# Optimization experiments

Hardware: AMD Instinct MI355X
Metric: run time of the kernel (lower is better)

The kernel has to match this reference:

```python
import jax, jax.numpy as jnp
import numpy as np

B, T, D = 4, 2048, 1024
H, Dh = 16, 64
Q_LAT, KV_LAT, O_LAT = 512, 256, 512
ROPE = 32
FFN_RANK, FFN_INTER = 384, 4096
EPS = 1e-6
THETA = 10000.0


def rms_norm(x, w, eps=EPS):
    xf = x.astype(jnp.float32)
    var = jnp.mean(xf * xf, axis=-1, keepdims=True)
    return (w * (xf * jax.lax.rsqrt(var + eps))).astype(x.dtype)


def rotate_half(x):
    x1, x2 = jnp.split(x, 2, axis=-1)
    return jnp.concatenate([-x2, x1], axis=-1)


def setup_inputs() -> dict:
    key = jax.random.key(0)
    ks = jax.random.split(key, 12)
    s = lambda fan_in: 1.0 / np.sqrt(fan_in)
    inp = {
        "hidden_states": jax.random.normal(ks[0], (B, T, D), jnp.float32),
        "ln1_w": jnp.ones((D,), jnp.float32),
        "a_ln_w": jnp.ones((Q_LAT + KV_LAT,), jnp.float32),
        "qkv_a_w": jax.random.normal(ks[1], (D, Q_LAT + KV_LAT), jnp.float32) * s(D),
        "q_b_w": jax.random.normal(ks[2], (Q_LAT, H * Dh), jnp.float32) * s(Q_LAT),
        "kv_b_w": jax.random.normal(ks[3], (KV_LAT, 2 * H * Dh), jnp.float32) * s(KV_LAT),
        "o_a_w": jax.random.normal(ks[4], (H * Dh, O_LAT), jnp.float32) * s(H * Dh),
        "o_b_w": jax.random.normal(ks[5], (O_LAT, D), jnp.float32) * s(O_LAT),
        "ln2_w": jnp.ones((D,), jnp.float32),
        "ffn_in_a": jax.random.normal(ks[6], (D, FFN_RANK), jnp.float32) * s(D),
        "ffn_in_b": jax.random.normal(ks[7], (FFN_RANK, FFN_INTER), jnp.float32) * s(FFN_RANK),
        "ffn_out_a": jax.random.normal(ks[8], (FFN_INTER, FFN_RANK), jnp.float32) * s(FFN_INTER),
        "ffn_out_b": jax.random.normal(ks[9], (FFN_RANK, D), jnp.float32) * s(FFN_RANK),
    }
    # RoPE tables over first ROPE dims of each head
    inv_freq = 1.0 / (THETA ** (np.arange(0, ROPE, 2, dtype=np.float32) / ROPE))
    t = np.arange(T, dtype=np.float32)
    freqs = np.outer(t, inv_freq)                      # [T, ROPE/2]
    emb = np.concatenate([freqs, freqs], axis=-1)      # [T, ROPE]
    inp["cos"] = jnp.asarray(np.cos(emb), jnp.float32)
    inp["sin"] = jnp.asarray(np.sin(emb), jnp.float32)
    return inp


def reference(hidden_states, cos, sin, ln1_w, a_ln_w, qkv_a_w, q_b_w, kv_b_w,
              o_a_w, o_b_w, ln2_w, ffn_in_a, ffn_in_b, ffn_out_a, ffn_out_b):
    x = hidden_states
    # --- MLA attention (pre-norm) ---
    h = rms_norm(x, ln1_w)
    lat = rms_norm(h @ qkv_a_w, a_ln_w)                # [B,T,Q_LAT+KV_LAT]
    q_lat, kv_lat = jnp.split(lat, [Q_LAT], axis=-1)
    q = (q_lat @ q_b_w).reshape(B, T, H, Dh).transpose(0, 2, 1, 3)   # [B,H,T,Dh]
    kv = (kv_lat @ kv_b_w).reshape(B, T, H, 2 * Dh).transpose(0, 2, 1, 3)
    k, v = jnp.split(kv, 2, axis=-1)
    # partial RoPE on first ROPE dims
    c = cos[None, None]; s_ = sin[None, None]          # [1,1,T,ROPE]
    q_r, q_p = q[..., :ROPE], q[..., ROPE:]
    k_r, k_p = k[..., :ROPE], k[..., ROPE:]
    q = jnp.concatenate([q_r * c + rotate_half(q_r) * s_, q_p], axis=-1)
    k = jnp.concatenate([k_r * c + rotate_half(k_r) * s_, k_p], axis=-1)
    scores = jnp.einsum("bhqd,bhkd->bhqk", q, k) * (Dh ** -0.5)
    attn = jax.nn.softmax(scores, axis=-1)
    ctx = jnp.einsum("bhqk,bhkd->bhqd", attn, v)
    ctx = ctx.transpose(0, 2, 1, 3).reshape(B, T, H * Dh)
    attn_out = (ctx @ o_a_w) @ o_b_w                   # output subspace
    x = x + attn_out
    # --- decomposed FFN (pre-norm) ---
    h2 = rms_norm(x, ln2_w)
    ff = jax.nn.gelu((h2 @ ffn_in_a) @ ffn_in_b)
    ff = (ff @ ffn_out_a) @ ffn_out_b
    return x + ff
```

## Files before the change

### kernel.cpp

```cpp
#include <hip/hip_runtime.h>
#include <hip/hip_bf16.h>
#include <stdint.h>

#define NTOK 8192

typedef unsigned short u16;
typedef __attribute__((ext_vector_type(4))) float f32x4;
typedef __attribute__((ext_vector_type(8))) short s16x8;
typedef __attribute__((ext_vector_type(4))) short s16x4;
typedef __attribute__((ext_vector_type(8))) u16   u16x8;
typedef __attribute__((ext_vector_type(4))) u16   u16x4;
typedef __attribute__((ext_vector_type(4))) uint32_t u32x4;

__device__ __forceinline__ float fast_exp2(float x) {
    return __builtin_amdgcn_exp2f(x);
}
__device__ __forceinline__ u16 f2bf(float f) {
    uint32_t u = __float_as_uint(f);
    u = (u + 0x7FFFu + ((u >> 16) & 1u)) >> 16;
    return (u16)u;
}
__device__ __forceinline__ float bf2f(u16 h) {
    return __uint_as_float(((uint32_t)h) << 16);
}
__device__ __forceinline__ void async_cp16(const void* g, void* l) {
    __builtin_amdgcn_global_load_lds(
        (const __attribute__((address_space(1))) void*)g,
        (__attribute__((address_space(3))) void*)l, 16, 0, 0);
}
__device__ __forceinline__ void wait_vm4()   { asm volatile("s_waitcnt vmcnt(4)" ::: "memory"); }
__device__ __forceinline__ void wait_vm0()   { asm volatile("s_waitcnt vmcnt(0)" ::: "memory"); }
__device__ __forceinline__ void wait_lgkm0() { asm volatile("s_waitcnt lgkmcnt(0)" ::: "memory"); }
__device__ __forceinline__ void raw_barrier(){ asm volatile("s_barrier" ::: "memory"); }

struct TDesc { const float* s; u16* d; int K; int N; int tile0; };
struct TPack { TDesc t[8]; };

__global__ __launch_bounds__(256) void k_transpose_all(TPack p)
{
    __shared__ float tile[32][33];
    int bid = blockIdx.x;
    int i = 0;
    #pragma unroll
    for (int j = 1; j < 8; j++) if (bid >= p.t[j].tile0) i = j;
    const float* src = p.t[i].s;
    u16* dst = p.t[i].d;
    int K = p.t[i].K, N = p.t[i].N;
    int local = bid - p.t[i].tile0;
    int nx = N >> 5;
    int n0 = (local % nx) * 32, k0 = (local / nx) * 32;
    int tx = threadIdx.x, ty = threadIdx.y;
    #pragma unroll
    for (int r = 0; r < 32; r += 8)
        tile[ty + r][tx] = src[(size_t)(k0 + ty + r) * N + n0 + tx];
    __syncthreads();
    #pragma unroll
    for (int r = 0; r < 32; r += 8)
        dst[(size_t)(n0 + ty + r) * K + k0 + tx] = f2bf(tile[tx][ty + r]);
}

__global__ __launch_bounds__(256) void k_cvt(
    const float* __restrict__ in, u16* __restrict__ out)
{
    int i = (blockIdx.x * 256 + threadIdx.x) * 4;
    f32x4 v = *(const f32x4*)&in[i];
    u16x4 o;
    #pragma unroll
    for (int j = 0; j < 4; j++) o[j] = f2bf(v[j]);
    *(u16x4*)&out[i] = o;
}

template<int W>
__global__ __launch_bounds__(256) void k_rmsnorm(
    const float* __restrict__ x, const float* __restrict__ w, u16* __restrict__ out)
{
    constexpr int E = W / 256;
    int row = blockIdx.x, tid = threadIdx.x;
    const float* xr = x + (size_t)row * W;
    float v[E]; float ss = 0.f;
    #pragma unroll
    for (int i = 0; i < E; i++) { v[i] = xr[tid + i * 256]; ss += v[i] * v[i]; }
    #pragma unroll
    for (int m = 1; m < 64; m <<= 1) ss += __shfl_xor(ss, m, 64);
    __shared__ float red[4];
    if ((tid & 63) == 0) red[tid >> 6] = ss;
    __syncthreads();
    ss = red[0] + red[1] + red[2] + red[3];
    float scale = rsqrtf(ss / (float)W + 1e-6f);
    u16* orow = out + (size_t)row * W;
    #pragma unroll
    for (int i = 0; i < E; i++)
        orow[tid + i * 256] = f2bf(w[tid + i * 256] * (v[i] * scale));
}

template<int EPI>
__global__ __launch_bounds__(256) void k_gemm(
    const u16* __restrict__ A, int lda,
    const u16* __restrict__ Bt, int ldb,
    int M, int N, int K,
    float* __restrict__ outF, u16* __restrict__ outB,
    const float* __restrict__ resid)
{
    __shared__ __align__(16) u16 As[2][4096];
    __shared__ __align__(16) u16 Bs[2][4096];
    int tid = threadIdx.x;
    int w = tid >> 6, lane = tid & 63;
    int m0 = blockIdx.y * 128, n0 = blockIdx.x * 128;
    int wm = w & 1, wn = w >> 1;
    int lr = lane & 15, lq = lane >> 4;

    f32x4 acc[4][4];
    #pragma unroll
    for (int i = 0; i < 4; i++)
        #pragma unroll
        for (int j = 0; j < 4; j++) acc[i][j] = (f32x4)(0.f);

    int ar = tid >> 2;
    int ac = (tid & 3) * 8;
    const u16* Ag = A  + (size_t)(m0 + ar) * lda + ac;
    const u16* Bg = Bt + (size_t)(n0 + ar) * ldb + ac;
    int lo = w * 512;

    auto stage = [&](int kt, int s) {
        const u16* a  = Ag + kt * 32;
        const u16* bp = Bg + kt * 32;
        async_cp16(a,                     &As[s][lo]);
        async_cp16(a + (size_t)64 * lda,  &As[s][lo + 2048]);
        async_cp16(bp,                    &Bs[s][lo]);
        async_cp16(bp + (size_t)64 * ldb, &Bs[s][lo + 2048]);
    };

    int nk = K >> 5;
    stage(0, 0);
    stage(1, 1);
    for (int k = 0; k < nk; k++) {
        if (k + 1 < nk) wait_vm4(); else wait_vm0();
        raw_barrier();
        int s = k & 1;
        s16x8 af[4], bfr[4];
        #pragma unroll
        for (int ms = 0; ms < 4; ms++)
            af[ms] = *reinterpret_cast<const s16x8*>(&As[s][(wm * 64 + ms * 16 + lr) * 32 + lq * 8]);
        #pragma unroll
        for (int ns = 0; ns < 4; ns++)
            bfr[ns] = *reinterpret_cast<const s16x8*>(&Bs[s][(wn * 64 + ns * 16 + lr) * 32 + lq * 8]);
        #pragma unroll
        for (int ms = 0; ms < 4; ms++)
            #pragma unroll
            for (int ns = 0; ns < 4; ns++)
                acc[ms][ns] = __builtin_amdgcn_mfma_f32_16x16x32_bf16(af[ms], bfr[ns], acc[ms][ns], 0, 0, 0);
        wait_lgkm0();
        raw_barrier();
        if (k + 2 < nk) stage(k + 2, s);
    }

    #pragma unroll
    for (int ms = 0; ms < 4; ms++) {
        #pragma unroll
        for (int ns = 0; ns < 4; ns++) {
            int col = n0 + wn * 64 + ns * 16 + lr;
            #pragma unroll
            for (int r = 0; r < 4; r++) {
                int row = m0 + wm * 64 + ms * 16 + lq * 4 + r;
                float v = acc[ms][ns][r];
                size_t idx = (size_t)row * N + col;
                if (EPI == 0) {
                    outF[idx] = v;
                } else if (EPI == 1) {
                    outB[idx] = f2bf(v);
                } else if (EPI == 2) {
                    float t = 0.7978845608028654f * (v + 0.044715f * v * v * v);
                    outB[idx] = f2bf(0.5f * v * (1.f + tanhf(t)));
                } else {
                    outF[idx] = v + resid[idx];
                }
            }
        }
    }
}

template<int EPI>
__global__ __launch_bounds__(256) void k_gemm64(
    const u16* __restrict__ A, int lda,
    const u16* __restrict__ Bt, int ldb,
    int M, int N, int K,
    float* __restrict__ outF, u16* __restrict__ outB)
{
    __shared__ __align__(16) u16 As[2][4096];
    __shared__ __align__(16) u16 Bs[2][4096];
    int tid = threadIdx.x;
    int w = tid >> 6, lane = tid & 63;
    int m0 = blockIdx.y * 64, n0 = blockIdx.x * 64;
    int wm = w & 1, wn = w >> 1;
    int lr = lane & 15, lq = lane >> 4;

    f32x4 acc[2][2];
    #pragma unroll
    for (int i = 0; i < 2; i++)
        #pragma unroll
        for (int j = 0; j < 2; j++) acc[i][j] = (f32x4)(0.f);

    int srow = tid >> 2;
    int sq   = tid & 3;
    const u16* Ag = A  + (size_t)(m0 + srow) * lda + sq * 8;
    const u16* Bg = Bt + (size_t)(n0 + srow) * ldb + sq * 8;
    int lo = srow * 32 + sq * 8;

    auto stage = [&](int kt, int s) {
        const u16* a  = Ag + kt * 64;
        const u16* bp = Bg + kt * 64;
        async_cp16(a,       &As[s][lo]);
        async_cp16(a + 32,  &As[s][2048 + lo]);
        async_cp16(bp,      &Bs[s][lo]);
        async_cp16(bp + 32, &Bs[s][2048 + lo]);
    };

    int nk = K >> 6;
    stage(0, 0);
    stage(1, 1);
    for (int k = 0; k < nk; k++) {
        if (k + 1 < nk) wait_vm4(); else wait_vm0();
        raw_barrier();
        int s = k & 1;
        s16x8 af[2][2], bfr[2][2];
        #pragma unroll
        for (int kc = 0; kc < 2; kc++) {
            #pragma unroll
            for (int ms = 0; ms < 2; ms++)
                af[ms][kc] = *reinterpret_cast<const s16x8*>(
                    &As[s][kc * 2048 + (wm * 32 + ms * 16 + lr) * 32 + lq * 8]);
            #pragma unroll
            for (int ns = 0; ns < 2; ns++)
                bfr[ns][kc] = *reinterpret_cast<const s16x8*>(
                    &Bs[s][kc * 2048 + (wn * 32 + ns * 16 + lr) * 32 + lq * 8]);
        }
        #pragma unroll
        for (int kc = 0; kc < 2; kc++)
            #pragma unroll
            for (int ms = 0; ms < 2; ms++)
                #pragma unroll
                for (int ns = 0; ns < 2; ns++)
                    acc[ms][ns] = __builtin_amdgcn_mfma_f32_16x16x32_bf16(
                        af[ms][kc], bfr[ns][kc], acc[ms][ns], 0, 0, 0);
        wait_lgkm0();
        raw_barrier();
        if (k + 2 < nk) stage(k + 2, s);
    }

    #pragma unroll
    for (int ms = 0; ms < 2; ms++) {
        #pragma unroll
        for (int ns = 0; ns < 2; ns++) {
            int col = n0 + wn * 32 + ns * 16 + lr;
            #pragma unroll
            for (int r = 0; r < 4; r++) {
                int row = m0 + wm * 32 + ms * 16 + lq * 4 + r;
                float v = acc[ms][ns][r];
                size_t idx = (size_t)row * N + col;
                if (EPI == 0) outF[idx] = v;
                else          outB[idx] = f2bf(v);
            }
        }
    }
}

__global__ __launch_bounds__(256) void k_rope(
    const u16* __restrict__ q, const u16* __restrict__ kv,
    const float* __restrict__ cosb, const float* __restrict__ sinb,
    u16* __restrict__ q_r, u16* __restrict__ k_r)
{
    const float QS = 0.125f * 1.4426950408889634f;
    int idx = blockIdx.x * 256 + threadIdx.x;
    int g = idx & 7;
    int h = (idx >> 3) & 15;
    int t = (idx >> 7) & 2047;
    int b = idx >> 18;
    size_t qsrc = ((size_t)((b * 2048 + t) * 16 + h)) * 64 + g * 8;
    size_t ksrc = ((size_t)((b * 2048 + t) * 16 + h)) * 128 + g * 8;
    u16x8 qa = *(const u16x8*)&q[qsrc];
    u16x8 ka = *(const u16x8*)&kv[ksrc];
    u16x8 qo, ko;
    if (g < 4) {
        int pd = ((g ^ 2) - g) * 8;
        u16x8 qp = *(const u16x8*)&q[qsrc + pd];
        u16x8 kp = *(const u16x8*)&kv[ksrc + pd];
        float sgn = (g < 2) ? -1.f : 1.f;
        const float* cp = &cosb[t * 32 + g * 8];
        const float* sp = &sinb[t * 32 + g * 8];
        #pragma unroll
        for (int j = 0; j < 8; j++) {
            float c = cp[j], s = sp[j];
            qo[j] = f2bf((bf2f(qa[j]) * c + sgn * bf2f(qp[j]) * s) * QS);
            ko[j] = f2bf(bf2f(ka[j]) * c + sgn * bf2f(kp[j]) * s);
        }
    } else {
        #pragma unroll
        for (int j = 0; j < 8; j++) {
            qo[j] = f2bf(bf2f(qa[j]) * QS);
            ko[j] = ka[j];
        }
    }
    size_t dst = ((size_t)(b * 16 + h) * 2048 + t) * 64 + g * 8;
    *(u16x8*)&q_r[dst] = qo;
    *(u16x8*)&k_r[dst] = ko;
}

__global__ __launch_bounds__(256) void k_vtrans(
    const u16* __restrict__ kv, u16* __restrict__ v_t)
{
    __shared__ u16 tile[64][72];
    int bh = blockIdx.y;
    int b = bh >> 4, h = bh & 15;
    int t0 = blockIdx.x * 64;
    int tid = threadIdx.x;
    int r = tid >> 2;
    int c4 = (tid & 3) * 16;
    const u16* src = kv + ((size_t)((b * 2048 + t0 + r) * 16 + h)) * 128 + 64;
    #pragma unroll
    for (int j = 0; j < 16; j += 8)
        *(u16x8*)&tile[r][c4 + j] = *(const u16x8*)&src[c4 + j];
    __syncthreads();
    int dd = tid >> 2;
    u16* dst = v_t + ((size_t)bh * 64 + dd) * 2048 + t0;
    #pragma unroll
    for (int j0 = 0; j0 < 16; j0 += 8) {
        u16x8 vv;
        #pragma unroll
        for (int j = 0; j < 8; j++) vv[j] = tile[c4 + j0 + j][dd];
        *(u16x8*)&dst[c4 + j0] = vv;
    }
}

__global__ __launch_bounds__(256) void k_attn(
    const u16* __restrict__ q_r, const u16* __restrict__ k_r,
    const u16* __restrict__ v_t, u16* __restrict__ ctx)
{
    __shared__ __align__(16) u16 Ks[2][4096];
    __shared__ __align__(16) u16 Vs[2][4096];
    int tid = threadIdx.x, w = tid >> 6, lane = tid & 63;
    int bh = blockIdx.y;
    int b = bh >> 4, h = bh & 15;
    int q0 = blockIdx.x * 128 + w * 32;
    const u16* Qp = q_r + (size_t)bh * 2048 * 64;
    const u16* Kp = k_r + (size_t)bh * 2048 * 64;
    const u16* Vp = v_t + (size_t)bh * 64 * 2048;
    int lr = lane & 15, lq = lane >> 4;
    int swz = (lr >> 1) & 3;

    s16x8 qf[2][2];
    #pragma unroll
    for (int qc = 0; qc < 2; qc++)
        #pragma unroll
        for (int kf = 0; kf < 2; kf++)
            qf[qc][kf] = *(const s16x8*)&Qp[(size_t)(q0 + qc * 16 + lr) * 64 + kf * 32 + lq * 8];

    s16x8 ones;
    #pragma unroll
    for (int j = 0; j < 8; j++) ones[j] = (short)0x3F80;

    int schunk = ((lane & 3) ^ ((lane >> 3) & 3)) * 8;
    const u16* gp;
    u16 *lp0, *lp1;
    size_t grow;
    int gAdv;
    if (w < 2) {
        gp = Kp + (size_t)(lane >> 2) * 64 + w * 32 + schunk;
        lp0 = &Ks[0][w * 2048]; lp1 = &Ks[1][w * 2048];
        grow = 16 * 64;  gAdv = 64 * 64;
    } else {
        gp = Vp + (size_t)(lane >> 2) * 2048 + (w - 2) * 32 + schunk;
        lp0 = &Vs[0][(w - 2) * 2048]; lp1 = &Vs[1][(w - 2) * 2048];
        grow = 16 * 2048; gAdv = 64;
    }
    auto stageP = [&](u16* lp) {
        #pragma unroll
        for (int g = 0; g < 4; g++)
            async_cp16(gp + g * grow, lp + g * 512);
        gp += gAdv;
    };

    f32x4 o[2][4];
    #pragma unroll
    for (int qt = 0; qt < 2; qt++)
        #pragma unroll
        for (int ds = 0; ds < 4; ds++) o[qt][ds] = (f32x4)(0.f);
    f32x4 lacc0 = (f32x4)(0.f), lacc1 = (f32x4)(0.f);

#define ATTN_BODY(S)                                                           \
  {                                                                            \
    f32x4 sc[2][4];                                                            \
    __builtin_amdgcn_s_setprio(1);                                             \
    _Pragma("unroll")                                                          \
    for (int ns = 0; ns < 4; ns++) {                                           \
      int ko = (ns * 16 + lr) * 32 + ((lq ^ swz) * 8);                         \
      s16x8 a0 = *(const s16x8*)&Ks[S][ko];                                    \
      s16x8 a1 = *(const s16x8*)&Ks[S][2048 + ko];                             \
      _Pragma("unroll")                                                        \
      for (int qc = 0; qc < 2; qc++) {                                         \
        f32x4 t = (f32x4)(0.f);                                                \
        t = __builtin_amdgcn_mfma_f32_16x16x32_bf16(a0, qf[qc][0], t, 0, 0, 0);\
        t = __builtin_amdgcn_mfma_f32_16x16x32_bf16(a1, qf[qc][1], t, 0, 0, 0);\
        sc[qc][ns] = t;                                                        \
      }                                                                        \
    }                                                                          \
    __builtin_amdgcn_s_setprio(0);                                             \
    _Pragma("unroll")                                                          \
    for (int kf = 0; kf < 2; kf++) {                                           \
      u32x4 w0, w1;                                                            \
      _Pragma("unroll")                                                        \
      for (int j = 0; j < 4; j++) {                                            \
        int ns = kf * 2 + (j >> 1);                                            \
        int r0 = (j & 1) * 2;                                                  \
        float ea = fast_exp2(sc[0][ns][r0]);                                   \
        float eb = fast_exp2(sc[0][ns][r0 + 1]);                               \
        float ec = fast_exp2(sc[1][ns][r0]);                                   \
        float ed = fast_exp2(sc[1][ns][r0 + 1]);                               \
        uint32_t t0, t1;                                                       \
        asm("v_cvt_pk_bf16_f32 %0, %1, %2" : "=v"(t0) : "v"(ea), "v"(eb));     \
        asm("v_cvt_pk_bf16_f32 %0, %1, %2" : "=v"(t1) : "v"(ec), "v"(ed));     \
        w0[j] = t0; w1[j] = t1;                                                \
      }                                                                        \
      s16x8 pk0 = __builtin_bit_cast(s16x8, w0);                               \
      s16x8 pk1 = __builtin_bit_cast(s16x8, w1);                               \
      __builtin_amdgcn_s_setprio(1);                                           \
      lacc0 = __builtin_amdgcn_mfma_f32_16x16x32_bf16(pk0, ones, lacc0, 0,0,0);\
      lacc1 = __builtin_amdgcn_mfma_f32_16x16x32_bf16(pk1, ones, lacc1, 0,0,0);\
      _Pragma("unroll")                                                        \
      for (int ds = 0; ds < 4; ds++) {                                         \
        int vbase = kf * 2048 + (ds * 16 + lr) * 32 + (lq & 1) * 4;            \
        s16x4 vlo = *(const s16x4*)&Vs[S][vbase + (((lq >> 1)    ) ^ swz) * 8];\
        s16x4 vhi = *(const s16x4*)&Vs[S][vbase + (((lq >> 1) | 2) ^ swz) * 8];\
        s16x8 vf = __builtin_shufflevector(vlo, vhi, 0, 1, 2, 3, 4, 5, 6, 7);  \
        o[0][ds] = __builtin_amdgcn_mfma_f32_16x16x32_bf16(pk0, vf, o[0][ds], 0, 0, 0);\
        o[1][ds] = __builtin_amdgcn_mfma_f32_16x16x32_bf16(pk1, vf, o[1][ds], 0, 0, 0);\
      }                                                                        \
      __builtin_amdgcn_s_setprio(0);                                           \
    }                                                                          \
  }

    stageP(lp0);
    stageP(lp1);
    for (int k2 = 0; k2 < 15; k2++) {
        wait_vm4(); raw_barrier();
        ATTN_BODY(0)
        wait_lgkm0(); raw_barrier();
        stageP(lp0);
        wait_vm4(); raw_barrier();
        ATTN_BODY(1)
        wait_lgkm0(); raw_barrier();
        stageP(lp1);
    }
    wait_vm4(); raw_barrier();
    ATTN_BODY(0)
    wait_vm0(); raw_barrier();
    ATTN_BODY(1)
#undef ATTN_BODY

    #pragma unroll
    for (int qt = 0; qt < 2; qt++) {
        f32x4 lv = qt ? lacc1 : lacc0;
        float li[4];
        #pragma unroll
        for (int r = 0; r < 4; r++) li[r] = 1.f / lv[r];
        #pragma unroll
        for (int ds = 0; ds < 4; ds++)
            #pragma unroll
            for (int r = 0; r < 4; r++) {
                int tq = q0 + qt * 16 + lq * 4 + r;
                float v = o[qt][ds][r] * li[r];
                ctx[((size_t)(b * 2048) + tq) * 1024 + h * 64 + ds * 16 + lr] = f2bf(v);
            }
    }
}

extern "C" void kernel_launch(void* const* d_in, const int* in_sizes, int n_in,
                              void* d_out, int out_size, void* d_ws, size_t ws_size,
                              hipStream_t stream) {
    (void)in_sizes; (void)n_in; (void)out_size; (void)ws_size;
    const float* x     = (const float*)d_in[0];
    const float* ln1   = (const float*)d_in[1];
    const float* alnw  = (const float*)d_in[2];
    const float* qkv_a = (const float*)d_in[3];
    const float* q_b   = (const float*)d_in[4];
    const float* kv_b  = (const float*)d_in[5];
    const float* o_a   = (const float*)d_in[6];
    const float* o_b   = (const float*)d_in[7];
    const float* ln2   = (const float*)d_in[8];
    const float* in_a  = (const float*)d_in[9];
    const float* in_b  = (const float*)d_in[10];
    const float* out_a = (const float*)d_in[11];
    const float* out_b = (const float*)d_in[12];
    const float* cosb  = (const float*)d_in[13];
    const float* sinb  = (const float*)d_in[14];
    float* out = (float*)d_out;
    char* ws = (char*)d_ws;

    u16* wqkv = (u16*)ws;
    u16* wq   = wqkv + 786432;
    u16* wkv  = wq   + 524288;
    u16* wob  = wkv  + 524288;
    u16* wia  = wob  + 524288;
    u16* wib  = wia  + 393216;
    u16* woa2 = wib  + 1572864;
    u16* wob2 = woa2 + 1572864;
    u16* woan = wob2 + 393216;
    u16* woab = woan + 524288;

    char* G = ws + 15728640;
    u16*  hbuf  = (u16*)(G + 0);
    float* lat_raw = (float*)(G + 16777216);
    u16*  lat   = (u16*)(G + 41943040);
    u16*  qbuf  = (u16*)(G + 54525952);
    u16*  kvbuf = (u16*)(G + 71303168);
    u16*  q_r   = (u16*)(G + 0);
    u16*  k_r   = (u16*)(G + 16777216);
    u16*  v_t   = (u16*)(G + 33554432);
    u16*  ctx   = (u16*)(G + 54525952);
    float* x2   = (float*)(G + 0);
    u16*  h2    = (u16*)(G + 33554432);
    u16*  t1    = (u16*)(G + 50331648);
    u16*  t2    = (u16*)(G + 56623104);
    u16*  t3    = (u16*)(G + 50331648);

    TPack tp;
    tp.t[0] = { qkv_a, wqkv, 1024, 768,  0 };
    tp.t[1] = { q_b,   wq,   512,  1024, 768 };
    tp.t[2] = { kv_b,  wkv,  256,  2048, 1280 };
    tp.t[3] = { o_b,   wob,  512,  1024, 1792 };
    tp.t[4] = { in_a,  wia,  1024, 384,  2304 };
    tp.t[5] = { in_b,  wib,  384,  4096, 2688 };
    tp.t[6] = { out_a, woa2, 4096, 384,  4224 };
    tp.t[7] = { out_b, wob2, 384,  1024, 5760 };
    k_transpose_all<<<6144, dim3(32, 8), 0, stream>>>(tp);
    k_cvt<<<512, 256, 0, stream>>>(o_a, woan);
    k_gemm64<1><<<dim3(16, 16), 256, 0, stream>>>(wob, 512, woan, 512, 1024, 1024, 512, nullptr, woab);

    k_rmsnorm<1024><<<NTOK, 256, 0, stream>>>(x, ln1, hbuf);
    k_gemm64<0><<<dim3(12, 128), 256, 0, stream>>>(hbuf, 1024, wqkv, 1024, NTOK, 768, 1024, lat_raw, nullptr);
    k_rmsnorm<768><<<NTOK, 256, 0, stream>>>(lat_raw, alnw, lat);
    k_gemm<1><<<dim3(8, 64),  256, 0, stream>>>(lat,       768, wq,  512, NTOK, 1024, 512, nullptr, qbuf,  nullptr);
    k_gemm<1><<<dim3(16, 64), 256, 0, stream>>>(lat + 512, 768, wkv, 256, NTOK, 2048, 256, nullptr, kvbuf, nullptr);
    k_rope<<<4096, 256, 0, stream>>>(qbuf, kvbuf, cosb, sinb, q_r, k_r);
    k_vtrans<<<dim3(32, 64), 256, 0, stream>>>(kvbuf, v_t);
    k_attn<<<dim3(16, 64), 256, 0, stream>>>(q_r, k_r, v_t, ctx);
    k_gemm<3><<<dim3(8, 64), 256, 0, stream>>>(ctx, 1024, woab, 1024, NTOK, 1024, 1024, x2, nullptr, x);
    k_rmsnorm<1024><<<NTOK, 256, 0, stream>>>(x2, ln2, h2);
    k_gemm64<1><<<dim3(6, 128), 256, 0, stream>>>(h2, 1024, wia, 1024, NTOK, 384, 1024, nullptr, t1);
    k_gemm<2><<<dim3(32, 64), 256, 0, stream>>>(t1, 384, wib, 384, NTOK, 4096, 384, nullptr, t2, nullptr);
    k_gemm64<1><<<dim3(6, 128), 256, 0, stream>>>(t2, 4096, woa2, 4096, NTOK, 384, 4096, nullptr, t3);
    k_gemm<3><<<dim3(8, 64), 256, 0, stream>>>(t3, 384, wob2, 384, NTOK, 1024, 384, out, nullptr, x2);
}
```

Before: 523.0 us.

## Remap attention blocks per XCD and batch V loads with ds_read2_b64

The attention grid is flattened and remapped so that all query blocks of the same batch-head land on the same XCD, which should improve L2 reuse of K and V. The LDS swizzle is narrowed, and the per-ds pairs of 64-bit V reads are replaced by four inline-asm ds_read2_b64 loads issued before the exp/pack work, so their latency is hidden. Other small tweaks: a zero accumulator hidden behind an opaque asm so the first MFMA skips materialising zeros, and a hardware rcp in place of division for the normaliser. The inline asm and the explicit lgkm wait with a sched_barrier constrain compiler scheduling, and the changed swizzle must stay consistent with the staging layout or it risks bank conflicts or wrong reads.

```diff
diff --git a/kernel.cpp b/kernel.cpp
--- a/kernel.cpp
+++ b/kernel.cpp
@@ -338,14 +338,18 @@
     __shared__ __align__(16) u16 Ks[2][4096];
     __shared__ __align__(16) u16 Vs[2][4096];
     int tid = threadIdx.x, w = tid >> 6, lane = tid & 63;
-    int bh = blockIdx.y;
+    int flat = blockIdx.x;
+    int xcd = flat & 7;
+    int idx = flat >> 3;
+    int bh  = xcd * 8 + (idx & 7);
+    int xb  = idx >> 3;
     int b = bh >> 4, h = bh & 15;
-    int q0 = blockIdx.x * 128 + w * 32;
+    int q0 = xb * 128 + w * 32;
     const u16* Qp = q_r + (size_t)bh * 2048 * 64;
     const u16* Kp = k_r + (size_t)bh * 2048 * 64;
     const u16* Vp = v_t + (size_t)bh * 64 * 2048;
     int lr = lane & 15, lq = lane >> 4;
-    int swz = (lr >> 1) & 3;
+    int swz = (lr >> 1) & 1;
 
     s16x8 qf[2][2];
     #pragma unroll
@@ -358,7 +362,10 @@
     #pragma unroll
     for (int j = 0; j < 8; j++) ones[j] = (short)0x3F80;
 
-    int schunk = ((lane & 3) ^ ((lane >> 3) & 3)) * 8;
+    f32x4 fz = (f32x4)(0.f);
+    asm("" : "+v"(fz));
+
+    int schunk = ((lane & 3) ^ ((lane >> 3) & 1)) * 8;
     const u16* gp;
     u16 *lp0, *lp1;
     size_t grow;
@@ -379,6 +386,9 @@
         gp += gAdv;
     };
 
+    uint32_t vaddr = (uint32_t)(uintptr_t)(&Vs[0][0])
+                   + (uint32_t)(lr * 64 + (lq & 1) * 8 + (((lq >> 1) ^ swz) * 16));
+
     f32x4 o[2][4];
     #pragma unroll
     for (int qt = 0; qt < 2; qt++)
@@ -397,8 +407,8 @@
       s16x8 a1 = *(const s16x8*)&Ks[S][2048 + ko];                             \
       _Pragma("unroll")                                                        \
       for (int qc = 0; qc < 2; qc++) {                                         \
-        f32x4 t = (f32x4)(0.f);                                                \
-        t = __builtin_amdgcn_mfma_f32_16x16x32_bf16(a0, qf[qc][0], t, 0, 0, 0);\
+        f32x4 t;                                                               \
+        t = __builtin_amdgcn_mfma_f32_16x16x32_bf16(a0, qf[qc][0], fz, 0, 0, 0);\
         t = __builtin_amdgcn_mfma_f32_16x16x32_bf16(a1, qf[qc][1], t, 0, 0, 0);\
         sc[qc][ns] = t;                                                        \
       }                                                                        \
@@ -406,6 +416,16 @@
     __builtin_amdgcn_s_setprio(0);                                             \
     _Pragma("unroll")                                                          \
     for (int kf = 0; kf < 2; kf++) {                                           \
+      uint32_t vaA = vaddr + ((S) * 8192 + kf * 4096);                         \
+      uint32_t vaB = vaA + 2048;                                               \
+      s16x8 vf0, vf1, vf2, vf3;                                                \
+      asm volatile(                                                            \
+        "ds_read2_b64 %0, %4 offset0:0 offset1:4\n\t"                          \
+        "ds_read2_b64 %1, %4 offset0:128 offset1:132\n\t"                      \
+        "ds_read2_b64 %2, %5 offset0:0 offset1:4\n\t"                          \
+        "ds_read2_b64 %3, %5 offset0:128 offset1:132"                          \
+        : "=v"(vf0), "=v"(vf1), "=v"(vf2), "=v"(vf3)                           \
+        : "v"(vaA), "v"(vaB));                                                 \
       u32x4 w0, w1;                                                            \
       _Pragma("unroll")                                                        \
       for (int j = 0; j < 4; j++) {                                            \
@@ -422,18 +442,19 @@
       }                                                                        \
       s16x8 pk0 = __builtin_bit_cast(s16x8, w0);                               \
       s16x8 pk1 = __builtin_bit_cast(s16x8, w1);                               \
+      wait_lgkm0();                                                            \
+      __builtin_amdgcn_sched_barrier(0);                                       \
       __builtin_amdgcn_s_setprio(1);                                           \
       lacc0 = __builtin_amdgcn_mfma_f32_16x16x32_bf16(pk0, ones, lacc0, 0,0,0);\
       lacc1 = __builtin_amdgcn_mfma_f32_16x16x32_bf16(pk1, ones, lacc1, 0,0,0);\
-      _Pragma("unroll")                                                        \
-      for (int ds = 0; ds < 4; ds++) {                                         \
-        int vbase = kf * 2048 + (ds * 16 + lr) * 32 + (lq & 1) * 4;            \
-        s16x4 vlo = *(const s16x4*)&Vs[S][vbase + (((lq >> 1)    ) ^ swz) * 8];\
-        s16x4 vhi = *(const s16x4*)&Vs[S][vbase + (((lq >> 1) | 2) ^ swz) * 8];\
-        s16x8 vf = __builtin_shufflevector(vlo, vhi, 0, 1, 2, 3, 4, 5, 6, 7);  \
-        o[0][ds] = __builtin_amdgcn_mfma_f32_16x16x32_bf16(pk0, vf, o[0][ds], 0, 0, 0);\
-        o[1][ds] = __builtin_amdgcn_mfma_f32_16x16x32_bf16(pk1, vf, o[1][ds], 0, 0, 0);\
-      }                                                                        \
+      o[0][0] = __builtin_amdgcn_mfma_f32_16x16x32_bf16(pk0, vf0, o[0][0], 0, 0, 0);\
+      o[1][0] = __builtin_amdgcn_mfma_f32_16x16x32_bf16(pk1, vf0, o[1][0], 0, 0, 0);\
+      o[0][1] = __builtin_amdgcn_mfma_f32_16x16x32_bf16(pk0, vf1, o[0][1], 0, 0, 0);\
+      o[1][1] = __builtin_amdgcn_mfma_f32_16x16x32_bf16(pk1, vf1, o[1][1], 0, 0, 0);\
+      o[0][2] = __builtin_amdgcn_mfma_f32_16x16x32_bf16(pk0, vf2, o[0][2], 0, 0, 0);\
+      o[1][2] = __builtin_amdgcn_mfma_f32_16x16x32_bf16(pk1, vf2, o[1][2], 0, 0, 0);\
+      o[0][3] = __builtin_amdgcn_mfma_f32_16x16x32_bf16(pk0, vf3, o[0][3], 0, 0, 0);\
+      o[1][3] = __builtin_amdgcn_mfma_f32_16x16x32_bf16(pk1, vf3, o[1][3], 0, 0, 0);\
       __builtin_amdgcn_s_setprio(0);                                           \
     }                                                                          \
   }
@@ -461,7 +482,7 @@
         f32x4 lv = qt ? lacc1 : lacc0;
         float li[4];
         #pragma unroll
-        for (int r = 0; r < 4; r++) li[r] = 1.f / lv[r];
+        for (int r = 0; r < 4; r++) li[r] = __builtin_amdgcn_rcpf(lv[r]);
         #pragma unroll
         for (int ds = 0; ds < 4; ds++)
             #pragma unroll
@@ -542,7 +563,7 @@
     k_gemm<1><<<dim3(16, 64), 256, 0, stream>>>(lat + 512, 768, wkv, 256, NTOK, 2048, 256, nullptr, kvbuf, nullptr);
     k_rope<<<4096, 256, 0, stream>>>(qbuf, kvbuf, cosb, sinb, q_r, k_r);
     k_vtrans<<<dim3(32, 64), 256, 0, stream>>>(kvbuf, v_t);
-    k_attn<<<dim3(16, 64), 256, 0, stream>>>(q_r, k_r, v_t, ctx);
+    k_attn<<<1024, 256, 0, stream>>>(q_r, k_r, v_t, ctx);
     k_gemm<3><<<dim3(8, 64), 256, 0, stream>>>(ctx, 1024, woab, 1024, NTOK, 1024, 1024, x2, nullptr, x);
     k_rmsnorm<1024><<<NTOK, 256, 0, stream>>>(x2, ln2, h2);
     k_gemm64<1><<<dim3(6, 128), 256, 0, stream>>>(h2, 1024, wia, 1024, NTOK, 384, 1024, nullptr, t1);
```

Result: slower. 539.1 us (+3.1%).
